# Kernel tuning notes

Measured on AMD Instinct MI355X. Metric: run time of the kernel, lower is better.

Reference implementation:

```python
import jax, jax.numpy as jnp
import numpy as np


def _sage(x_src, x_dst, src, dst, Wl, bl, Wr, n_dst):
    # gather source features along edges, mean-aggregate into destinations
    m = x_src[src]                                              # [E, H]
    s = jax.ops.segment_sum(m, dst, num_segments=n_dst)        # [N_dst, H]
    cnt = jax.ops.segment_sum(jnp.ones(src.shape, x_src.dtype), dst, num_segments=n_dst)
    mean = s / jnp.maximum(cnt, 1.0)[:, None]
    # SAGEConv: lin_l(agg) + lin_r(x_dst)  (lin_r has no bias in PyG)
    return mean @ Wl + bl + x_dst @ Wr


def setup_inputs() -> dict:
    key = jax.random.key(0)
    ks = jax.random.split(key, 24)
    N_C, N_T, E = 100000, 5000, 2000000
    D_C, D_T, H, H2 = 1024, 1280, 64, 32
    s = 0.05  # weight scale to keep residual stack numerically tame
    inp = {
        "x_comp": jax.random.normal(ks[0], (N_C, D_C), jnp.float32),
        "x_tgt": jax.random.normal(ks[1], (N_T, D_T), jnp.float32),
        "src_ct": jax.random.randint(ks[2], (E,), 0, N_C, jnp.int32),
        "dst_ct": jax.random.randint(ks[3], (E,), 0, N_T, jnp.int32),
        "src_tc": jax.random.randint(ks[4], (E,), 0, N_T, jnp.int32),
        "dst_tc": jax.random.randint(ks[5], (E,), 0, N_C, jnp.int32),
        "Wc": jax.random.normal(ks[6], (D_C, H), jnp.float32) * s,
        "bc": jax.random.normal(ks[7], (H,), jnp.float32) * s,
        "Wt": jax.random.normal(ks[8], (D_T, H), jnp.float32) * s,
        "bt": jax.random.normal(ks[9], (H,), jnp.float32) * s,
        "Wl_ct": jax.random.normal(ks[10], (3, H, H), jnp.float32) * s,
        "bl_ct": jax.random.normal(ks[11], (3, H), jnp.float32) * s,
        "Wr_ct": jax.random.normal(ks[12], (3, H, H), jnp.float32) * s,
        "Wl_tc": jax.random.normal(ks[13], (3, H, H), jnp.float32) * s,
        "bl_tc": jax.random.normal(ks[14], (3, H), jnp.float32) * s,
        "Wr_tc": jax.random.normal(ks[15], (3, H, H), jnp.float32) * s,
        "Wo1": jax.random.normal(ks[16], (H, H2), jnp.float32) * s,
        "bo1": jax.random.normal(ks[17], (H2,), jnp.float32) * s,
        "Wo2": jax.random.normal(ks[18], (H2, 1), jnp.float32) * s,
        "bo2": jax.random.normal(ks[19], (1,), jnp.float32) * s,
    }
    return inp


def reference(x_comp, x_tgt, src_ct, dst_ct, src_tc, dst_tc,
              Wc, bc, Wt, bt,
              Wl_ct, bl_ct, Wr_ct, Wl_tc, bl_tc, Wr_tc,
              Wo1, bo1, Wo2, bo2):
    xc = jax.nn.relu(x_comp @ Wc + bc)   # [N_C, H]
    xt = jax.nn.relu(x_tgt @ Wt + bt)    # [N_T, H]
    n_layers = Wl_ct.shape[0]
    for l in range(n_layers):
        # compound -> target updates targets; target -> compound updates compounds
        new_t = _sage(xc, xt, src_ct, dst_ct, Wl_ct[l], bl_ct[l], Wr_ct[l], xt.shape[0])
        new_c = _sage(xt, xc, src_tc, dst_tc, Wl_tc[l], bl_tc[l], Wr_tc[l], xc.shape[0])
        xc = jax.nn.relu(new_c) + xc
        xt = jax.nn.relu(new_t) + xt
    # output head on compounds (dropout is identity in eval)
    h = jax.nn.relu(xc @ Wo1 + bo1)
    return h @ Wo2 + bo2
```

## Files before the change

kernel.cpp:

```cpp
#include <hip/hip_runtime.h>

typedef unsigned int uint32;
typedef __bf16 bf16x8 __attribute__((ext_vector_type(8)));
typedef float f32x4 __attribute__((ext_vector_type(4)));

constexpr int N_C = 100000, N_T = 5000, E_EDGES = 2000000;
constexpr int D_C = 1024, D_T = 1280, H = 64, H2 = 32, NL = 3;
constexpr int PJC = (N_C + 63) / 64;
constexpr int PJT = (N_T + 63) / 64;
constexpr int NBC64 = (N_C + 63) / 64;

constexpr int CCH = 200;
constexpr int CHE = E_EDGES / CCH;
constexpr int SH_T = 4,  FB_T = 16;
constexpr int SH_C = 8,  FB_C = 256;
constexpr int NB_T_B = (N_T + FB_T - 1) / FB_T;
constexpr int NB_C_B = (N_C + FB_C - 1) / FB_C;
constexpr int NB_TOT = NB_T_B + NB_C_B;
constexpr int PB_T = 17; constexpr uint32 PM_T = 0x1FFFFu;
constexpr int PB_C = 13; constexpr uint32 PM_C = 0x1FFFu;

__device__ inline unsigned short f2bf(float f) {
  uint32 u = __float_as_uint(f);
  u += 0x7fffu + ((u >> 16) & 1u);
  return (unsigned short)(u >> 16);
}

__global__ __launch_bounds__(256) void prep_kernel(
    const float* __restrict__ Wc, const float* __restrict__ Wt,
    const float* __restrict__ Wl, const float* __restrict__ Wr,
    __bf16* __restrict__ WcT, __bf16* __restrict__ WtT, __bf16* __restrict__ WsT,
    int* __restrict__ T)
{
  int t = blockIdx.x * 256 + threadIdx.x;
  const int Z = NB_TOT;
  const int A = D_C * 64;
  const int B = D_T * 64;
  const int S = 6 * 64 * 64;
  if (t < Z) { T[t] = 0; return; }
  t -= Z;
  if (t < A) { int n = t & 63, k = t >> 6; WcT[(size_t)n * D_C + k] = (__bf16)Wc[(size_t)k * 64 + n]; return; }
  t -= A;
  if (t < B) { int n = t & 63, k = t >> 6; WtT[(size_t)n * D_T + k] = (__bf16)Wt[(size_t)k * 64 + n]; return; }
  t -= B;
  if (t < S) {
    int i = t >> 12;
    int r = t & 4095; int n = r & 63, k = r >> 6;
    const float* src = (i < 3) ? (Wl + (size_t)i * 4096) : (Wr + (size_t)(i - 3) * 4096);
    WsT[(size_t)i * 4096 + (size_t)n * 64 + k] = (__bf16)src[(size_t)k * 64 + n];
  }
}

template<int K>
__device__ __forceinline__ void projM16_body(
    const float* __restrict__ x, const __bf16* __restrict__ WT,
    const float* __restrict__ b, float* __restrict__ y,
    unsigned short* __restrict__ yh, int n, int bidx)
{
  int w = threadIdx.x >> 6, l = threadIdx.x & 63;
  int lm = l & 15, lk = l >> 4;
  int base = bidx * 64 + w * 16;
  int r0 = base + lm; if (r0 >= n) r0 = n - 1;
  const float* xp0 = x + (size_t)r0 * K + lk * 8;
  const __bf16* wp = WT + (size_t)lm * K + lk * 8;

  f32x4 acc[4] = {{0,0,0,0},{0,0,0,0},{0,0,0,0},{0,0,0,0}};

  float4 p0 = *(const float4*)(xp0);
  float4 p1 = *(const float4*)(xp0 + 4);
  float4 q0 = *(const float4*)(xp0 + 32);
  float4 q1 = *(const float4*)(xp0 + 36);

  for (int k0 = 0; k0 < K; k0 += 32) {
    bf16x8 a0;
    a0[0]=(__bf16)p0.x; a0[1]=(__bf16)p0.y; a0[2]=(__bf16)p0.z; a0[3]=(__bf16)p0.w;
    a0[4]=(__bf16)p1.x; a0[5]=(__bf16)p1.y; a0[6]=(__bf16)p1.z; a0[7]=(__bf16)p1.w;
    p0 = q0; p1 = q1;
    if (k0 + 64 < K) {
      q0 = *(const float4*)(xp0 + k0 + 64);
      q1 = *(const float4*)(xp0 + k0 + 68);
    }
#pragma unroll
    for (int fn = 0; fn < 4; ++fn) {
      bf16x8 bv = *(const bf16x8*)(wp + (size_t)fn * 16 * K + k0);
      acc[fn] = __builtin_amdgcn_mfma_f32_16x16x32_bf16(a0, bv, acc[fn], 0, 0, 0);
    }
  }

#pragma unroll
  for (int fn = 0; fn < 4; ++fn) {
    int col = fn * 16 + lm;
    float bb = b[col];
#pragma unroll
    for (int reg = 0; reg < 4; ++reg) {
      int row = base + lk * 4 + reg;
      if (row < n) {
        float o = fmaxf(acc[fn][reg] + bb, 0.f);
        y[(size_t)row * 64 + col] = o;
        yh[(size_t)row * 64 + col] = f2bf(o);
      }
    }
  }
}

__global__ __launch_bounds__(256) void proj_kernel(
    const float* __restrict__ x_comp, const __bf16* __restrict__ WcT,
    const float* __restrict__ bc, float* __restrict__ xc, unsigned short* __restrict__ xch,
    const float* __restrict__ x_tgt, const __bf16* __restrict__ WtT,
    const float* __restrict__ bt, float* __restrict__ xt, unsigned short* __restrict__ xth)
{
  if (blockIdx.x < PJC) projM16_body<D_C>(x_comp, WcT, bc, xc, xch, N_C, blockIdx.x);
  else                  projM16_body<D_T>(x_tgt, WtT, bt, xt, xth, N_T, blockIdx.x - PJC);
}

__global__ __launch_bounds__(256) void csr1_kernel(
    const int* __restrict__ dst_ct, const int* __restrict__ dst_tc,
    int* __restrict__ h1, int* __restrict__ T)
{
  __shared__ int hist[NB_C_B];
  int graph = (blockIdx.x >= CCH) ? 1 : 0;
  int chunk = graph ? (blockIdx.x - CCH) : blockIdx.x;
  const int* dst = graph ? dst_tc : dst_ct;
  int NB = graph ? NB_C_B : NB_T_B;
  int SH = graph ? SH_C : SH_T;
  for (int i = threadIdx.x; i < NB; i += 256) hist[i] = 0;
  __syncthreads();
  int e0 = chunk * CHE;
  for (int i = threadIdx.x; i < CHE; i += 256)
    atomicAdd(&hist[dst[e0 + i] >> SH], 1);
  __syncthreads();
  int* h1g = h1 + (graph ? (size_t)NB_T_B * CCH : 0);
  int* Tg  = T + (graph ? NB_T_B : 0);
  for (int i = threadIdx.x; i < NB; i += 256) {
    int v = hist[i];
    h1g[(size_t)i * CCH + chunk] = v;
    if (v) atomicAdd(&Tg[i], v);
  }
}

__global__ __launch_bounds__(256) void csr2_kernel(
    const int* __restrict__ h1, const int* __restrict__ T, int* __restrict__ b1)
{
  __shared__ int sh[256];
  __shared__ int loc2[512];
  int b = blockIdx.x;
  int graph = (b >= NB_T_B) ? 1 : 0;
  int nb = graph ? NB_C_B : NB_T_B;
  int base = graph ? NB_T_B : 0;
  int bl = b - base;
  int tid = threadIdx.x;
  int v0 = (2 * tid     < nb) ? T[base + 2 * tid]     : 0;
  int v1 = (2 * tid + 1 < nb) ? T[base + 2 * tid + 1] : 0;
  int t = v0 + v1;
  sh[tid] = t;
  __syncthreads();
  for (int off = 1; off < 256; off <<= 1) {
    int xv = (tid >= off) ? sh[tid - off] : 0;
    __syncthreads(); sh[tid] += xv; __syncthreads();
  }
  int excl = sh[tid] - t;
  loc2[2 * tid] = excl;
  loc2[2 * tid + 1] = excl + v0;
  __syncthreads();
  int B = loc2[bl];
  const int* row = h1 + (graph ? (size_t)NB_T_B * CCH : 0) + (size_t)bl * CCH;
  int hv = (tid < CCH) ? row[tid] : 0;
  sh[tid] = hv;
  __syncthreads();
  for (int off = 1; off < 256; off <<= 1) {
    int xv = (tid >= off) ? sh[tid - off] : 0;
    __syncthreads(); sh[tid] += xv; __syncthreads();
  }
  int e2 = sh[tid] - hv;
  if (tid < CCH) {
    int* b1g = b1 + (graph ? (size_t)NB_T_B * CCH : 0) + (size_t)bl * CCH;
    b1g[tid] = B + e2;
  }
}

__global__ __launch_bounds__(256) void csr3_kernel(
    const int* __restrict__ src_ct, const int* __restrict__ dst_ct,
    const int* __restrict__ src_tc, const int* __restrict__ dst_tc,
    const int* __restrict__ b1, uint32* __restrict__ packT_t, uint32* __restrict__ packT_c)
{
  __shared__ int cur[NB_C_B];
  int graph = (blockIdx.x >= CCH) ? 1 : 0;
  int chunk = graph ? (blockIdx.x - CCH) : blockIdx.x;
  const int* dst = graph ? dst_tc : dst_ct;
  const int* src = graph ? src_tc : src_ct;
  uint32* packT = graph ? packT_c : packT_t;
  int NB = graph ? NB_C_B : NB_T_B;
  int SH = graph ? SH_C : SH_T;
  int SB = graph ? PB_C : PB_T;
  const int* b1g = b1 + (graph ? (size_t)NB_T_B * CCH : 0);
  for (int i = threadIdx.x; i < NB; i += 256) cur[i] = b1g[(size_t)i * CCH + chunk];
  __syncthreads();
  int e0 = chunk * CHE;
  for (int i = threadIdx.x; i < CHE; i += 256) {
    int d = dst[e0 + i], s = src[e0 + i];
    int p = atomicAdd(&cur[d >> SH], 1);
    packT[p] = ((uint32)d << SB) | (uint32)s;
  }
}

__global__ __launch_bounds__(256) void csr4_kernel(
    const int* __restrict__ b1, const uint32* __restrict__ packT_t,
    const uint32* __restrict__ packT_c,
    int* __restrict__ rowptr_t, int* __restrict__ col_ct,
    int* __restrict__ rowptr_c, int* __restrict__ col_tc)
{
  __shared__ int hist[FB_C];
  __shared__ int exc[256];
  int b = blockIdx.x;
  int graph = (b >= NB_T_B) ? 1 : 0;
  int bl = graph ? (b - NB_T_B) : b;
  int nb = graph ? NB_C_B : NB_T_B;
  int FB = graph ? FB_C : FB_T;
  int SB = graph ? PB_C : PB_T;
  uint32 SM = graph ? PM_C : PM_T;
  uint32 FMM = (uint32)(FB - 1);
  int N  = graph ? N_C : N_T;
  const uint32* packT = graph ? packT_c : packT_t;
  int* rowptr = graph ? rowptr_c : rowptr_t;
  int* col    = graph ? col_tc : col_ct;
  const int* b1g = b1 + (graph ? (size_t)NB_T_B * CCH : 0);
  int seg0 = b1g[(size_t)bl * CCH];
  int seg1 = (bl + 1 < nb) ? b1g[(size_t)(bl + 1) * CCH] : E_EDGES;
  int tid = threadIdx.x;
  if (tid < FB) hist[tid] = 0;
  __syncthreads();
  for (int i = seg0 + tid; i < seg1; i += 256)
    atomicAdd(&hist[(packT[i] >> SB) & FMM], 1);
  __syncthreads();
  int hv = (tid < FB) ? hist[tid] : 0;
  exc[tid] = hv;
  __syncthreads();
  for (int off = 1; off < 256; off <<= 1) {
    int xv = (tid >= off) ? exc[tid - off] : 0;
    __syncthreads(); exc[tid] += xv; __syncthreads();
  }
  int excl = exc[tid] - hv;
  __syncthreads();
  if (tid < FB) {
    int gbin = bl * FB + tid;
    if (gbin <= N) rowptr[gbin] = seg0 + excl;
    hist[tid] = seg0 + excl;
  }
  __syncthreads();
  for (int i = seg0 + tid; i < seg1; i += 256) {
    uint32 pk = packT[i];
    int p = atomicAdd(&hist[(pk >> SB) & FMM], 1);
    col[p] = (int)(pk & SM);
  }
}

__global__ __launch_bounds__(256) void layerT_kernel(
    const unsigned short* __restrict__ xch_a, const float* __restrict__ xt_a,
    const int* __restrict__ rowptr_t, const int* __restrict__ col_ct,
    const float* __restrict__ Wl_t, const float* __restrict__ bl_t, const float* __restrict__ Wr_t,
    float* __restrict__ xt_n, unsigned short* __restrict__ xth_n)
{
  __shared__ __align__(16) float part[4][64];
  __shared__ __align__(16) float opart[4][64];

  int l = threadIdx.x & 63, w = threadIdx.x >> 6;
  int d = l & 31, half = l >> 5;

  int r = blockIdx.x;
  int start = rowptr_t[r], end = rowptr_t[r + 1];
  int deg = end - start;
  int quarter = (deg + 3) >> 2;
  int js = start + w * quarter;
  int je = js + quarter; if (je > end) je = end;
  const uint32* xp = (const uint32*)xch_a;
  float a0 = 0.f, a1 = 0.f;
  int j0 = js + half;
  for (int j = j0; j < je; j += 16) {
    int idx[8]; uint32 vv[8];
#pragma unroll
    for (int k = 0; k < 8; ++k) {
      int jj = j + 2 * k;
      idx[k] = col_ct[(jj < je) ? jj : j];
    }
#pragma unroll
    for (int k = 0; k < 8; ++k) vv[k] = xp[(size_t)idx[k] * 32 + d];
#pragma unroll
    for (int k = 0; k < 8; ++k) {
      bool m = (j + 2 * k) < je;
      a0 += m ? __uint_as_float(vv[k] << 16) : 0.f;
      a1 += m ? __uint_as_float(vv[k] & 0xffff0000u) : 0.f;
    }
  }
  a0 += __shfl_xor(a0, 32, 64);
  a1 += __shfl_xor(a1, 32, 64);
  if (half == 0) *(float2*)&part[w][2 * d] = make_float2(a0, a1);
  __syncthreads();
  float m = (part[0][l] + part[1][l] + part[2][l] + part[3][l])
            * ((deg > 0) ? (1.0f / (float)deg) : 0.f);
  float xv = xt_a[(size_t)r * 64 + l];
  float o = 0.f;
  int k0 = w * 16;
#pragma unroll
  for (int kk = 0; kk < 16; ++kk) {
    int k = k0 + kk;
    float mk = __uint_as_float(__builtin_amdgcn_readlane(__float_as_uint(m), k));
    float xk = __uint_as_float(__builtin_amdgcn_readlane(__float_as_uint(xv), k));
    o = fmaf(mk, Wl_t[k * 64 + l], o);
    o = fmaf(xk, Wr_t[k * 64 + l], o);
  }
  opart[w][l] = o;
  __syncthreads();
  if (w == 0) {
    float oo = opart[0][l] + opart[1][l] + opart[2][l] + opart[3][l] + bl_t[l];
    float res = fmaxf(oo, 0.f) + xv;
    xt_n[(size_t)r * 64 + l] = res;
    xth_n[(size_t)r * 64 + l] = f2bf(res);
  }
}

__global__ __launch_bounds__(256) void layerC_kernel(
    const unsigned short* __restrict__ xch_a,
    const unsigned short* __restrict__ xth_a, const int* __restrict__ rowptr_c,
    const int* __restrict__ col_tc,
    const __bf16* __restrict__ WlT, const __bf16* __restrict__ WrT,
    const float* __restrict__ bl_c, const float* __restrict__ xc_a,
    float* __restrict__ xc_n, unsigned short* __restrict__ xch_n)
{
  __shared__ __align__(16) uint32 smem_u[64 * 36];

  int l = threadIdx.x & 63, w = threadIdx.x >> 6;
  int d = l & 31, half = l >> 5;

  int bbase = blockIdx.x * 64;

  int rp_idx = bbase + w * 16 + ((l <= 16) ? l : 16);
  if (rp_idx > N_C) rp_idx = N_C;
  int rpl = rowptr_c[rp_idx];
  const uint32* xp = (const uint32*)xth_a;

#pragma unroll 1
  for (int t = 0; t < 8; ++t) {
    int s = __shfl(rpl, 2 * t + half, 64);
    int e = __shfl(rpl, 2 * t + half + 1, 64);
    float a0 = 0.f, a1 = 0.f;
    int n = e - s;
    for (int j = 0; j < n; j += 8) {
      int idx[8]; uint32 vv[8];
#pragma unroll
      for (int k = 0; k < 8; ++k) {
        int jj = s + j + k;
        idx[k] = col_tc[(jj < e) ? jj : s];
      }
#pragma unroll
      for (int k = 0; k < 8; ++k) vv[k] = xp[(size_t)idx[k] * 32 + d];
#pragma unroll
      for (int k = 0; k < 8; ++k) {
        bool m = (j + k) < n;
        a0 += m ? __uint_as_float(vv[k] << 16) : 0.f;
        a1 += m ? __uint_as_float(vv[k] & 0xffff0000u) : 0.f;
      }
    }
    float inv = (n > 0) ? (1.0f / (float)n) : 0.f;
    uint32 packed = (uint32)f2bf(a0 * inv) | ((uint32)f2bf(a1 * inv) << 16);
    smem_u[(size_t)(w * 16 + 2 * t + half) * 36 + d] = packed;
  }
  __syncthreads();

  int lm = l & 15, lk = l >> 4;
  int base = bbase + w * 16;
  int r0 = base + lm; if (r0 >= N_C) r0 = N_C - 1;
  const unsigned short* x0 = xch_a + (size_t)r0 * 64 + lk * 8;
  const __bf16* wl = WlT + (size_t)lm * 64 + lk * 8;
  const __bf16* wr = WrT + (size_t)lm * 64 + lk * 8;

  f32x4 acc[4] = {{0,0,0,0},{0,0,0,0},{0,0,0,0},{0,0,0,0}};

#pragma unroll
  for (int ks = 0; ks < 64; ks += 32) {
    bf16x8 am0 = *(const bf16x8*)&smem_u[(size_t)(w * 16 + lm) * 36 + lk * 4 + (ks >> 1)];
    bf16x8 ax0 = *(const bf16x8*)(x0 + ks);
#pragma unroll
    for (int fn = 0; fn < 4; ++fn) {
      bf16x8 bl_v = *(const bf16x8*)(wl + (size_t)fn * 16 * 64 + ks);
      bf16x8 br_v = *(const bf16x8*)(wr + (size_t)fn * 16 * 64 + ks);
      acc[fn] = __builtin_amdgcn_mfma_f32_16x16x32_bf16(am0, bl_v, acc[fn], 0, 0, 0);
      acc[fn] = __builtin_amdgcn_mfma_f32_16x16x32_bf16(ax0, br_v, acc[fn], 0, 0, 0);
    }
  }

#pragma unroll
  for (int fn = 0; fn < 4; ++fn) {
    int col = fn * 16 + lm;
    float bb = bl_c[col];
#pragma unroll
    for (int reg = 0; reg < 4; ++reg) {
      int row = base + lk * 4 + reg;
      if (row < N_C) {
        float xv = xc_a[(size_t)row * 64 + col];
        float o = fmaxf(acc[fn][reg] + bb, 0.f) + xv;
        xc_n[(size_t)row * 64 + col] = o;
        xch_n[(size_t)row * 64 + col] = f2bf(o);
      }
    }
  }
}

__global__ __launch_bounds__(256) void head_kernel(
    const float* __restrict__ xc, const float* __restrict__ Wo1,
    const float* __restrict__ bo1, const float* __restrict__ Wo2,
    const float* __restrict__ bo2, float* __restrict__ out, int n)
{
  int lane = threadIdx.x & 63;
  int wid = blockIdx.x * (blockDim.x >> 6) + (threadIdx.x >> 6);
  if (wid >= n) return;
  float xv = xc[(size_t)wid * 64 + lane];
  float h = (lane < H2) ? bo1[lane] : 0.f;
  const float* wcol = Wo1 + ((lane < H2) ? lane : 0);
#pragma unroll 8
  for (int k = 0; k < 64; ++k) {
    float xk = __uint_as_float(__builtin_amdgcn_readlane(__float_as_uint(xv), k));
    h = fmaf(xk, wcol[k * H2], h);
  }
  float v = (lane < H2) ? fmaxf(h, 0.f) * Wo2[lane] : 0.f;
#pragma unroll
  for (int off = 32; off > 0; off >>= 1) v += __shfl_down(v, off, 64);
  if (lane == 0) out[wid] = v + bo2[0];
}

extern "C" void kernel_launch(void* const* d_in, const int* in_sizes, int n_in,
                              void* d_out, int out_size, void* d_ws, size_t ws_size,
                              hipStream_t stream)
{
  const float* x_comp = (const float*)d_in[0];
  const float* x_tgt  = (const float*)d_in[1];
  const int*   src_ct = (const int*)d_in[2];
  const int*   dst_ct = (const int*)d_in[3];
  const int*   src_tc = (const int*)d_in[4];
  const int*   dst_tc = (const int*)d_in[5];
  const float* Wc    = (const float*)d_in[6];
  const float* bc    = (const float*)d_in[7];
  const float* Wt    = (const float*)d_in[8];
  const float* bt    = (const float*)d_in[9];
  const float* Wl_ct = (const float*)d_in[10];
  const float* bl_ct = (const float*)d_in[11];
  const float* Wr_ct = (const float*)d_in[12];
  const float* Wl_tc = (const float*)d_in[13];
  const float* bl_tc = (const float*)d_in[14];
  const float* Wr_tc = (const float*)d_in[15];
  const float* Wo1   = (const float*)d_in[16];
  const float* bo1   = (const float*)d_in[17];
  const float* Wo2   = (const float*)d_in[18];
  const float* bo2   = (const float*)d_in[19];
  float* out = (float*)d_out;

  char* p = (char*)d_ws;
  auto alloc = [&](size_t bytes) {
    char* q = p;
    p += (bytes + 255) & ~(size_t)255;
    return q;
  };
  float* xc   = (float*)alloc((size_t)N_C * H * 4);
  float* xt   = (float*)alloc((size_t)N_T * H * 4);
  float* xc_b = (float*)alloc((size_t)N_C * H * 4);
  float* xt_b = (float*)alloc((size_t)N_T * H * 4);
  unsigned short* xch   = (unsigned short*)alloc((size_t)N_C * H * 2);
  unsigned short* xth   = (unsigned short*)alloc((size_t)N_T * H * 2);
  unsigned short* xch_b = (unsigned short*)alloc((size_t)N_C * H * 2);
  unsigned short* xth_b = (unsigned short*)alloc((size_t)N_T * H * 2);
  __bf16* WcT = (__bf16*)alloc((size_t)D_C * H * 2);
  __bf16* WtT = (__bf16*)alloc((size_t)D_T * H * 2);
  __bf16* WsT = (__bf16*)alloc((size_t)6 * H * H * 2);
  int*    h1        = (int*)alloc((size_t)NB_TOT * CCH * 4);
  int*    b1        = (int*)alloc((size_t)NB_TOT * CCH * 4);
  int*    T         = (int*)alloc((size_t)NB_TOT * 4);
  uint32* packT_t   = (uint32*)alloc((size_t)E_EDGES * 4);
  uint32* packT_c   = (uint32*)alloc((size_t)E_EDGES * 4);
  int*    rowptr_t  = (int*)alloc((size_t)(N_T + 1) * 4);
  int*    rowptr_c  = (int*)alloc((size_t)(N_C + 1) * 4);
  int*    col_ct    = (int*)alloc((size_t)E_EDGES * 4);
  int*    col_tc    = (int*)alloc((size_t)E_EDGES * 4);

  const int PREP_TOTAL = NB_TOT + D_C * 64 + D_T * 64 + 6 * 4096;
  prep_kernel<<<dim3((PREP_TOTAL + 255) / 256), dim3(256), 0, stream>>>(
      Wc, Wt, Wl_tc, Wr_tc, WcT, WtT, WsT, T);

  proj_kernel<<<dim3(PJC + PJT), dim3(256), 0, stream>>>(
      x_comp, WcT, bc, xc, xch, x_tgt, WtT, bt, xt, xth);

  csr1_kernel<<<dim3(2 * CCH), dim3(256), 0, stream>>>(dst_ct, dst_tc, h1, T);
  csr2_kernel<<<dim3(NB_TOT), dim3(256), 0, stream>>>(h1, T, b1);
  csr3_kernel<<<dim3(2 * CCH), dim3(256), 0, stream>>>(
      src_ct, dst_ct, src_tc, dst_tc, b1, packT_t, packT_c);
  csr4_kernel<<<dim3(NB_TOT), dim3(256), 0, stream>>>(
      b1, packT_t, packT_c, rowptr_t, col_ct, rowptr_c, col_tc);

  float* xc_a = xc; float* xt_a = xt;
  float* xc_n = xc_b; float* xt_n = xt_b;
  unsigned short* xch_a = xch; unsigned short* xth_a = xth;
  unsigned short* xch_n = xch_b; unsigned short* xth_n = xth_b;
  for (int l = 0; l < NL; ++l) {
    layerT_kernel<<<dim3(N_T), dim3(256), 0, stream>>>(
        xch_a, xt_a, rowptr_t, col_ct,
        Wl_ct + (size_t)l * H * H, bl_ct + (size_t)l * H, Wr_ct + (size_t)l * H * H,
        xt_n, xth_n);
    layerC_kernel<<<dim3(NBC64), dim3(256), 0, stream>>>(
        xch_a, xth_a, rowptr_c, col_tc,
        WsT + (size_t)l * H * H, WsT + (size_t)(3 + l) * H * H,
        bl_tc + (size_t)l * H, xc_a, xc_n, xch_n);
    float* t;
    t = xc_a; xc_a = xc_n; xc_n = t;
    t = xt_a; xt_a = xt_n; xt_n = t;
    unsigned short* th;
    th = xch_a; xch_a = xch_n; xch_n = th;
    th = xth_a; xth_a = xth_n; xth_n = th;
  }

  head_kernel<<<dim3((N_C + 3) / 4), dim3(256), 0, stream>>>(xc_a, Wo1, bo1, Wo2, bo2, out, N_C);
}
```

Measured before the change: 655.9 us.

## Split-K projection across waves and vectorize compound-side edge gather

The input projection now assigns 16 rows per block and splits the K dimension across the four waves, then reduces the partial accumulators through shared memory. This gives four times as many blocks, for more parallelism and memory-level concurrency on the large dense read. The compound layer aggregation now has 8 lanes gather one edge's 128-byte row with 16-byte loads, so each wave handles 8 edges at once, followed by a cross-lane shuffle reduction. The cost is extra shared memory, a block sync, and shuffle reductions.

```diff
diff --git a/kernel.cpp b/kernel.cpp
--- a/kernel.cpp
+++ b/kernel.cpp
@@ -6,8 +6,8 @@
 
 constexpr int N_C = 100000, N_T = 5000, E_EDGES = 2000000;
 constexpr int D_C = 1024, D_T = 1280, H = 64, H2 = 32, NL = 3;
-constexpr int PJC = (N_C + 63) / 64;
-constexpr int PJT = (N_T + 63) / 64;
+constexpr int PJC = (N_C + 15) / 16;
+constexpr int PJT = (N_T + 15) / 16;
 constexpr int NBC64 = (N_C + 63) / 64;
 
 constexpr int CCH = 200;
@@ -52,33 +52,36 @@
 }
 
 template<int K>
-__device__ __forceinline__ void projM16_body(
+__device__ __forceinline__ void projKS_body(
     const float* __restrict__ x, const __bf16* __restrict__ WT,
     const float* __restrict__ b, float* __restrict__ y,
     unsigned short* __restrict__ yh, int n, int bidx)
 {
+  constexpr int KW = K / 4;
+  __shared__ __align__(16) float accL[4][16][65];
+
   int w = threadIdx.x >> 6, l = threadIdx.x & 63;
   int lm = l & 15, lk = l >> 4;
-  int base = bidx * 64 + w * 16;
+  int base = bidx * 16;
   int r0 = base + lm; if (r0 >= n) r0 = n - 1;
-  const float* xp0 = x + (size_t)r0 * K + lk * 8;
-  const __bf16* wp = WT + (size_t)lm * K + lk * 8;
+  const float* xp = x + (size_t)r0 * K + (size_t)w * KW + lk * 8;
+  const __bf16* wp = WT + (size_t)lm * K + (size_t)w * KW + lk * 8;
 
   f32x4 acc[4] = {{0,0,0,0},{0,0,0,0},{0,0,0,0},{0,0,0,0}};
 
-  float4 p0 = *(const float4*)(xp0);
-  float4 p1 = *(const float4*)(xp0 + 4);
-  float4 q0 = *(const float4*)(xp0 + 32);
-  float4 q1 = *(const float4*)(xp0 + 36);
-
-  for (int k0 = 0; k0 < K; k0 += 32) {
+  float4 p0 = *(const float4*)(xp);
+  float4 p1 = *(const float4*)(xp + 4);
+  float4 q0 = *(const float4*)(xp + 32);
+  float4 q1 = *(const float4*)(xp + 36);
+
+  for (int k0 = 0; k0 < KW; k0 += 32) {
     bf16x8 a0;
     a0[0]=(__bf16)p0.x; a0[1]=(__bf16)p0.y; a0[2]=(__bf16)p0.z; a0[3]=(__bf16)p0.w;
     a0[4]=(__bf16)p1.x; a0[5]=(__bf16)p1.y; a0[6]=(__bf16)p1.z; a0[7]=(__bf16)p1.w;
     p0 = q0; p1 = q1;
-    if (k0 + 64 < K) {
-      q0 = *(const float4*)(xp0 + k0 + 64);
-      q1 = *(const float4*)(xp0 + k0 + 68);
+    if (k0 + 64 < KW) {
+      q0 = *(const float4*)(xp + k0 + 64);
+      q1 = *(const float4*)(xp + k0 + 68);
     }
 #pragma unroll
     for (int fn = 0; fn < 4; ++fn) {
@@ -88,17 +91,21 @@
   }
 
 #pragma unroll
-  for (int fn = 0; fn < 4; ++fn) {
-    int col = fn * 16 + lm;
-    float bb = b[col];
-#pragma unroll
-    for (int reg = 0; reg < 4; ++reg) {
-      int row = base + lk * 4 + reg;
-      if (row < n) {
-        float o = fmaxf(acc[fn][reg] + bb, 0.f);
-        y[(size_t)row * 64 + col] = o;
-        yh[(size_t)row * 64 + col] = f2bf(o);
-      }
+  for (int fn = 0; fn < 4; ++fn)
+#pragma unroll
+    for (int reg = 0; reg < 4; ++reg)
+      accL[w][lk * 4 + reg][fn * 16 + lm] = acc[fn][reg];
+  __syncthreads();
+
+#pragma unroll
+  for (int rr = 0; rr < 4; ++rr) {
+    int lr = w * 4 + rr;
+    int row = base + lr;
+    if (row < n) {
+      float s = accL[0][lr][l] + accL[1][lr][l] + accL[2][lr][l] + accL[3][lr][l] + b[l];
+      float o = fmaxf(s, 0.f);
+      y[(size_t)row * 64 + l] = o;
+      yh[(size_t)row * 64 + l] = f2bf(o);
     }
   }
 }
@@ -109,8 +116,8 @@
     const float* __restrict__ x_tgt, const __bf16* __restrict__ WtT,
     const float* __restrict__ bt, float* __restrict__ xt, unsigned short* __restrict__ xth)
 {
-  if (blockIdx.x < PJC) projM16_body<D_C>(x_comp, WcT, bc, xc, xch, N_C, blockIdx.x);
-  else                  projM16_body<D_T>(x_tgt, WtT, bt, xt, xth, N_T, blockIdx.x - PJC);
+  if (blockIdx.x < PJC) projKS_body<D_C>(x_comp, WcT, bc, xc, xch, N_C, blockIdx.x);
+  else                  projKS_body<D_T>(x_tgt, WtT, bt, xt, xth, N_T, blockIdx.x - PJC);
 }
 
 __global__ __launch_bounds__(256) void csr1_kernel(
@@ -329,40 +336,52 @@
   __shared__ __align__(16) uint32 smem_u[64 * 36];
 
   int l = threadIdx.x & 63, w = threadIdx.x >> 6;
-  int d = l & 31, half = l >> 5;
+  int g = l >> 3, q = l & 7;
 
   int bbase = blockIdx.x * 64;
 
   int rp_idx = bbase + w * 16 + ((l <= 16) ? l : 16);
   if (rp_idx > N_C) rp_idx = N_C;
   int rpl = rowptr_c[rp_idx];
-  const uint32* xp = (const uint32*)xth_a;
+  const uint4* xp4 = (const uint4*)xth_a;
 
 #pragma unroll 1
-  for (int t = 0; t < 8; ++t) {
-    int s = __shfl(rpl, 2 * t + half, 64);
-    int e = __shfl(rpl, 2 * t + half + 1, 64);
-    float a0 = 0.f, a1 = 0.f;
-    int n = e - s;
-    for (int j = 0; j < n; j += 8) {
-      int idx[8]; uint32 vv[8];
-#pragma unroll
-      for (int k = 0; k < 8; ++k) {
-        int jj = s + j + k;
-        idx[k] = col_tc[(jj < e) ? jj : s];
+  for (int t = 0; t < 16; ++t) {
+    int s = __shfl(rpl, t, 64);
+    int e = __shfl(rpl, t + 1, 64);
+    int deg = e - s;
+    float a[8] = {0.f,0.f,0.f,0.f,0.f,0.f,0.f,0.f};
+    for (int j = s; j < e; j += 32) {
+#pragma unroll
+      for (int bb = 0; bb < 4; ++bb) {
+        int ej = j + bb * 8 + g;
+        int cc = col_tc[(ej < e) ? ej : j];
+        uint4 v = xp4[(size_t)cc * 8 + q];
+        bool m = ej < e;
+        a[0] += m ? __uint_as_float(v.x << 16) : 0.f;
+        a[1] += m ? __uint_as_float(v.x & 0xffff0000u) : 0.f;
+        a[2] += m ? __uint_as_float(v.y << 16) : 0.f;
+        a[3] += m ? __uint_as_float(v.y & 0xffff0000u) : 0.f;
+        a[4] += m ? __uint_as_float(v.z << 16) : 0.f;
+        a[5] += m ? __uint_as_float(v.z & 0xffff0000u) : 0.f;
+        a[6] += m ? __uint_as_float(v.w << 16) : 0.f;
+        a[7] += m ? __uint_as_float(v.w & 0xffff0000u) : 0.f;
       }
-#pragma unroll
-      for (int k = 0; k < 8; ++k) vv[k] = xp[(size_t)idx[k] * 32 + d];
-#pragma unroll
-      for (int k = 0; k < 8; ++k) {
-        bool m = (j + k) < n;
-        a0 += m ? __uint_as_float(vv[k] << 16) : 0.f;
-        a1 += m ? __uint_as_float(vv[k] & 0xffff0000u) : 0.f;
+    }
+#pragma unroll
+    for (int i = 0; i < 8; ++i) a[i] += __shfl_xor(a[i], 8, 64);
+#pragma unroll
+    for (int i = 0; i < 8; ++i) a[i] += __shfl_xor(a[i], 16, 64);
+#pragma unroll
+    for (int i = 0; i < 8; ++i) a[i] += __shfl_xor(a[i], 32, 64);
+    if (g == 0) {
+      float inv = (deg > 0) ? (1.0f / (float)deg) : 0.f;
+#pragma unroll
+      for (int i = 0; i < 4; ++i) {
+        uint32 pk = (uint32)f2bf(a[2 * i] * inv) | ((uint32)f2bf(a[2 * i + 1] * inv) << 16);
+        smem_u[(size_t)(w * 16 + t) * 36 + q * 4 + i] = pk;
       }
     }
-    float inv = (n > 0) ? (1.0f / (float)n) : 0.f;
-    uint32 packed = (uint32)f2bf(a0 * inv) | ((uint32)f2bf(a1 * inv) << 16);
-    smem_u[(size_t)(w * 16 + 2 * t + half) * 36 + d] = packed;
   }
   __syncthreads();
 
```

Measured after the change: 749.9 us. +14.3%, slower.

## Stage projection input tiles through LDS and pre-swizzle weights into MFMA fragment order

Applied to the files above, without the earlier changes.

The input projection now loads each 64-row by 128-column fp32 tile cooperatively with coalesced float4 reads, converts it to bf16 and stores it in padded shared memory. MFMA A-fragments are then read from LDS. The weight prep kernel rewrites Wc and Wt into a fragment-major layout so each lane reads its B operand as one contiguous 16-byte load. This targets the strided per-lane global reads of x in the old kernel, which read the 400 MB x_comp poorly. In exchange it adds block barriers and LDS traffic per tile, and drops the register prefetch that overlapped loads with compute.

```diff
diff --git a/kernel.cpp b/kernel.cpp
--- a/kernel.cpp
+++ b/kernel.cpp
@@ -2,6 +2,7 @@
 
 typedef unsigned int uint32;
 typedef __bf16 bf16x8 __attribute__((ext_vector_type(8)));
+typedef __bf16 bf16x4 __attribute__((ext_vector_type(4)));
 typedef float f32x4 __attribute__((ext_vector_type(4)));
 
 constexpr int N_C = 100000, N_T = 5000, E_EDGES = 2000000;
@@ -29,7 +30,7 @@
 __global__ __launch_bounds__(256) void prep_kernel(
     const float* __restrict__ Wc, const float* __restrict__ Wt,
     const float* __restrict__ Wl, const float* __restrict__ Wr,
-    __bf16* __restrict__ WcT, __bf16* __restrict__ WtT, __bf16* __restrict__ WsT,
+    __bf16* __restrict__ WfC, __bf16* __restrict__ WfT, __bf16* __restrict__ WsT,
     int* __restrict__ T)
 {
   int t = blockIdx.x * 256 + threadIdx.x;
@@ -39,9 +40,21 @@
   const int S = 6 * 64 * 64;
   if (t < Z) { T[t] = 0; return; }
   t -= Z;
-  if (t < A) { int n = t & 63, k = t >> 6; WcT[(size_t)n * D_C + k] = (__bf16)Wc[(size_t)k * 64 + n]; return; }
+  if (t < A) {
+    int j = t & 7, l = (t >> 3) & 63, frag = t >> 9;
+    int k0 = (frag >> 2) * 32, fn = frag & 3;
+    int lm = l & 15, lk = l >> 4;
+    WfC[t] = (__bf16)Wc[(size_t)(k0 + lk * 8 + j) * 64 + fn * 16 + lm];
+    return;
+  }
   t -= A;
-  if (t < B) { int n = t & 63, k = t >> 6; WtT[(size_t)n * D_T + k] = (__bf16)Wt[(size_t)k * 64 + n]; return; }
+  if (t < B) {
+    int j = t & 7, l = (t >> 3) & 63, frag = t >> 9;
+    int k0 = (frag >> 2) * 32, fn = frag & 3;
+    int lm = l & 15, lk = l >> 4;
+    WfT[t] = (__bf16)Wt[(size_t)(k0 + lk * 8 + j) * 64 + fn * 16 + lm];
+    return;
+  }
   t -= B;
   if (t < S) {
     int i = t >> 12;
@@ -52,38 +65,53 @@
 }
 
 template<int K>
-__device__ __forceinline__ void projM16_body(
-    const float* __restrict__ x, const __bf16* __restrict__ WT,
+__device__ __forceinline__ void projLDS_body(
+    const float* __restrict__ x, const __bf16* __restrict__ Wf,
     const float* __restrict__ b, float* __restrict__ y,
     unsigned short* __restrict__ yh, int n, int bidx)
 {
-  int w = threadIdx.x >> 6, l = threadIdx.x & 63;
+  constexpr int NT = K / 128;
+  constexpr int ST = 152;
+  __shared__ __align__(16) __bf16 sA[64 * ST];
+
+  int t = threadIdx.x;
+  int w = t >> 6, l = t & 63;
   int lm = l & 15, lk = l >> 4;
-  int base = bidx * 64 + w * 16;
-  int r0 = base + lm; if (r0 >= n) r0 = n - 1;
-  const float* xp0 = x + (size_t)r0 * K + lk * 8;
-  const __bf16* wp = WT + (size_t)lm * K + lk * 8;
+  int bbase = bidx * 64;
+  int rowbase = bbase + w * 16;
 
   f32x4 acc[4] = {{0,0,0,0},{0,0,0,0},{0,0,0,0},{0,0,0,0}};
 
-  float4 p0 = *(const float4*)(xp0);
-  float4 p1 = *(const float4*)(xp0 + 4);
-  float4 q0 = *(const float4*)(xp0 + 32);
-  float4 q1 = *(const float4*)(xp0 + 36);
-
-  for (int k0 = 0; k0 < K; k0 += 32) {
-    bf16x8 a0;
-    a0[0]=(__bf16)p0.x; a0[1]=(__bf16)p0.y; a0[2]=(__bf16)p0.z; a0[3]=(__bf16)p0.w;
-    a0[4]=(__bf16)p1.x; a0[5]=(__bf16)p1.y; a0[6]=(__bf16)p1.z; a0[7]=(__bf16)p1.w;
-    p0 = q0; p1 = q1;
-    if (k0 + 64 < K) {
-      q0 = *(const float4*)(xp0 + k0 + 64);
-      q1 = *(const float4*)(xp0 + k0 + 68);
-    }
-#pragma unroll
-    for (int fn = 0; fn < 4; ++fn) {
-      bf16x8 bv = *(const bf16x8*)(wp + (size_t)fn * 16 * K + k0);
-      acc[fn] = __builtin_amdgcn_mfma_f32_16x16x32_bf16(a0, bv, acc[fn], 0, 0, 0);
+  int srow = t >> 5;
+  int sc4  = t & 31;
+
+  for (int tile = 0; tile < NT; ++tile) {
+    if (tile) __syncthreads();
+    float4 g[8];
+#pragma unroll
+    for (int r = 0; r < 8; ++r) {
+      int row = srow + r * 8;
+      int gr = bbase + row; if (gr >= n) gr = n - 1;
+      g[r] = *(const float4*)(x + (size_t)gr * K + tile * 128 + sc4 * 4);
+    }
+#pragma unroll
+    for (int r = 0; r < 8; ++r) {
+      int row = srow + r * 8;
+      bf16x4 v;
+      v[0] = (__bf16)g[r].x; v[1] = (__bf16)g[r].y;
+      v[2] = (__bf16)g[r].z; v[3] = (__bf16)g[r].w;
+      *(bf16x4*)(sA + (size_t)row * ST + sc4 * 4) = v;
+    }
+    __syncthreads();
+
+#pragma unroll
+    for (int kk = 0; kk < 4; ++kk) {
+      bf16x8 a0 = *(const bf16x8*)(sA + (size_t)(w * 16 + lm) * ST + kk * 32 + lk * 8);
+#pragma unroll
+      for (int fn = 0; fn < 4; ++fn) {
+        bf16x8 bv = *(const bf16x8*)(Wf + ((size_t)(tile * 4 + kk) * 4 + fn) * 512 + l * 8);
+        acc[fn] = __builtin_amdgcn_mfma_f32_16x16x32_bf16(a0, bv, acc[fn], 0, 0, 0);
+      }
     }
   }
 
@@ -93,7 +121,7 @@
     float bb = b[col];
 #pragma unroll
     for (int reg = 0; reg < 4; ++reg) {
-      int row = base + lk * 4 + reg;
+      int row = rowbase + lk * 4 + reg;
       if (row < n) {
         float o = fmaxf(acc[fn][reg] + bb, 0.f);
         y[(size_t)row * 64 + col] = o;
@@ -104,13 +132,13 @@
 }
 
 __global__ __launch_bounds__(256) void proj_kernel(
-    const float* __restrict__ x_comp, const __bf16* __restrict__ WcT,
+    const float* __restrict__ x_comp, const __bf16* __restrict__ WfC,
     const float* __restrict__ bc, float* __restrict__ xc, unsigned short* __restrict__ xch,
-    const float* __restrict__ x_tgt, const __bf16* __restrict__ WtT,
+    const float* __restrict__ x_tgt, const __bf16* __restrict__ WfT,
     const float* __restrict__ bt, float* __restrict__ xt, unsigned short* __restrict__ xth)
 {
-  if (blockIdx.x < PJC) projM16_body<D_C>(x_comp, WcT, bc, xc, xch, N_C, blockIdx.x);
-  else                  projM16_body<D_T>(x_tgt, WtT, bt, xt, xth, N_T, blockIdx.x - PJC);
+  if (blockIdx.x < PJC) projLDS_body<D_C>(x_comp, WfC, bc, xc, xch, N_C, blockIdx.x);
+  else                  projLDS_body<D_T>(x_tgt, WfT, bt, xt, xth, N_T, blockIdx.x - PJC);
 }
 
 __global__ __launch_bounds__(256) void csr1_kernel(
@@ -467,8 +495,8 @@
   unsigned short* xth   = (unsigned short*)alloc((size_t)N_T * H * 2);
   unsigned short* xch_b = (unsigned short*)alloc((size_t)N_C * H * 2);
   unsigned short* xth_b = (unsigned short*)alloc((size_t)N_T * H * 2);
-  __bf16* WcT = (__bf16*)alloc((size_t)D_C * H * 2);
-  __bf16* WtT = (__bf16*)alloc((size_t)D_T * H * 2);
+  __bf16* WfC = (__bf16*)alloc((size_t)D_C * H * 2);
+  __bf16* WfT = (__bf16*)alloc((size_t)D_T * H * 2);
   __bf16* WsT = (__bf16*)alloc((size_t)6 * H * H * 2);
   int*    h1        = (int*)alloc((size_t)NB_TOT * CCH * 4);
   int*    b1        = (int*)alloc((size_t)NB_TOT * CCH * 4);
@@ -482,10 +510,10 @@
 
   const int PREP_TOTAL = NB_TOT + D_C * 64 + D_T * 64 + 6 * 4096;
   prep_kernel<<<dim3((PREP_TOTAL + 255) / 256), dim3(256), 0, stream>>>(
-      Wc, Wt, Wl_tc, Wr_tc, WcT, WtT, WsT, T);
+      Wc, Wt, Wl_tc, Wr_tc, WfC, WfT, WsT, T);
 
   proj_kernel<<<dim3(PJC + PJT), dim3(256), 0, stream>>>(
-      x_comp, WcT, bc, xc, xch, x_tgt, WtT, bt, xt, xth);
+      x_comp, WfC, bc, xc, xch, x_tgt, WfT, bt, xt, xth);
 
   csr1_kernel<<<dim3(2 * CCH), dim3(256), 0, stream>>>(dst_ct, dst_tc, h1, T);
   csr2_kernel<<<dim3(NB_TOT), dim3(256), 0, stream>>>(h1, T, b1);
```

Measured after the change: 598.4 us (median of 2 runs). 1.1x faster.
